# Kernel tuning notes

Hardware: AMD Instinct MI355X
Metric: run time of the kernel (lower is better)

Reference implementation:

```python
import jax, jax.numpy as jnp
import numpy as np

B, H, I = 16384, 512, 256
EPS = 1e-8

def setup_inputs() -> dict:
    key = jax.random.key(0)
    ks = jax.random.split(key, 10)
    x = jax.random.normal(ks[0], (B, I), dtype=jnp.float32)
    hx_re = jax.random.normal(ks[1], (B, H), dtype=jnp.float32) * 0.05
    hx_im = jax.random.normal(ks[2], (B, H), dtype=jnp.float32) * 0.05
    # diag = exp(1j * U(-pi, pi)) -> store angles as real params
    diag_angles = jax.random.uniform(ks[3], (3 * H,), dtype=jnp.float32,
                                     minval=-np.pi, maxval=np.pi)
    # rotation = U(0,1)*2 - (1+1j): real part in [-1,1], imag part in [-1,1]
    rot_re = jax.random.uniform(ks[4], (2 * H,), dtype=jnp.float32) * 2.0 - 1.0
    rot_im = jax.random.uniform(ks[5], (2 * H,), dtype=jnp.float32) * 2.0 - 1.0
    # xavier-scale complex Linear weight (hidden, input), no bias
    w_scale = float(np.sqrt(2.0 / (I + H)))
    W_re = jax.random.normal(ks[6], (H, I), dtype=jnp.float32) * w_scale
    W_im = jax.random.normal(ks[7], (H, I), dtype=jnp.float32) * w_scale
    beta = jnp.zeros((H,), dtype=jnp.float32)  # ModReLU bias, zeros init
    perm = jax.random.permutation(ks[8], H).astype(jnp.int32)
    return {"x": x, "hx_re": hx_re, "hx_im": hx_im,
            "diag_angles": diag_angles, "rot_re": rot_re, "rot_im": rot_im,
            "W_re": W_re, "W_im": W_im, "beta": beta, "perm": perm}

def _unit(v):
    # complex_unit_norm: v / (||v|| + eps), norm over last dim
    return v / (jnp.linalg.norm(v) + EPS)

def _apply_householder(h, v):
    # h @ (I - 2 v v^H) == h - 2 (h @ v) v^H  (rank-1 form, no NxN matrix)
    return h - 2.0 * (h @ v)[:, None] * jnp.conj(v)[None, :]

def reference(x, hx_re, hx_im, diag_angles, rot_re, rot_im, W_re, W_im, beta, perm):
    diag = jnp.exp(1j * diag_angles)                 # complex64, |.| = 1
    d1, d2, d3 = jnp.split(diag, 3)
    rot = rot_re + 1j * rot_im
    r1, r2 = jnp.split(rot, 2)
    v1 = _unit(r1)
    v2 = _unit(r2)

    h = hx_re + 1j * hx_im                           # (B, H) complex64
    h = jnp.fft.fft(d1[None, :] * h, axis=-1)        # D1 then F
    h = _apply_householder(h, v1)                    # R1
    h = jnp.fft.ifft(d2[None, :] * h[:, perm], axis=-1)  # Pi, D2, F^-1
    h = d3[None, :] * _apply_householder(h, v2)      # R2 then D3
    # complex Linear on real input: x @ W^T with complex W
    emb = (x @ W_re.T) + 1j * (x @ W_im.T)
    h = h + emb
    # ModReLU: relu(|z| + beta) * exp(1j * angle(z))
    mag = jnp.abs(h)
    out = jax.nn.relu(mag + beta[None, :]) * jnp.exp(1j * jnp.angle(h))
    # return as real (B, H, 2) [real, imag] for real-valued harness
    return jnp.stack([out.real, out.imag], axis=-1)
```

## Files before the change

kernel.cpp:

```cpp
#include <hip/hip_runtime.h>
#include <hip/hip_bf16.h>
#include <stdint.h>
#include <stddef.h>

typedef __bf16 bf16;
typedef bf16 bf16x8 __attribute__((ext_vector_type(8)));
typedef float f32x4 __attribute__((ext_vector_type(4)));

#define EPSN 1e-8f
#define TWO_PI 6.283185307179586f

#define NB 16384
#define NH 512
#define NI 256
#define KTOT 1280
#define NKT 20

__device__ __forceinline__ float2 cmul(float2 a, float2 b) {
  return make_float2(a.x * b.x - a.y * b.y, a.x * b.y + a.y * b.x);
}
__device__ __forceinline__ float2 cmulconj(float2 a, float2 b) {
  return make_float2(a.x * b.x + a.y * b.y, a.y * b.x - a.x * b.y);
}
__device__ __forceinline__ float2 cadd(float2 a, float2 b) {
  return make_float2(a.x + b.x, a.y + b.y);
}
__device__ __forceinline__ int brev9(int i) {
  return (int)(__brev((unsigned)i) >> 23);
}

__device__ __forceinline__ void gload16(const bf16* g, bf16* l) {
  __builtin_amdgcn_global_load_lds(
      (const __attribute__((address_space(1))) void*)g,
      (__attribute__((address_space(3))) void*)l, 16, 0, 0);
}

__global__ __launch_bounds__(256) void prep(
    const float* __restrict__ ang, const float* __restrict__ rre,
    const float* __restrict__ rim, const float* __restrict__ wre,
    const float* __restrict__ wim, const int* __restrict__ perm,
    const float* __restrict__ hxre, const float* __restrict__ hxim,
    const float* __restrict__ x, bf16* __restrict__ Bm,
    bf16* __restrict__ Apack) {
  __shared__ float2 bufA[512];
  __shared__ float2 bufB[512];
  __shared__ float2 redw[4];
  __shared__ float2 bc;
  __shared__ float2 red2[256];

  const int bid = blockIdx.x;
  const int t = threadIdx.x;

  if (bid >= 512) {
    const int tid = (bid - 512) * 256 + t;
    const int b = tid / 160;
    const int o = tid - b * 160;
    const float* src;
    if (o < 64)
      src = hxre + (size_t)b * 512 + o * 8;
    else if (o < 128)
      src = hxim + (size_t)b * 512 + (o - 64) * 8;
    else
      src = x + (size_t)b * 256 + (o - 128) * 8;
    float4 f0 = ((const float4*)src)[0];
    float4 f1 = ((const float4*)src)[1];
    bf16x8 v;
    v[0] = (bf16)f0.x; v[1] = (bf16)f0.y; v[2] = (bf16)f0.z; v[3] = (bf16)f0.w;
    v[4] = (bf16)f1.x; v[5] = (bf16)f1.y; v[6] = (bf16)f1.z; v[7] = (bf16)f1.w;
    *(bf16x8*)(Apack + (size_t)b * KTOT + o * 8) = v;
    return;
  }

  const int j = bid;
  const int j0 = t, j1 = t + 256;

  const float r1x0 = rre[j0], r1y0 = rim[j0];
  const float r1x1 = rre[j1], r1y1 = rim[j1];
  const float r2x0 = rre[512 + j0], r2y0 = rim[512 + j0];
  const float r2x1 = rre[512 + j1], r2y1 = rim[512 + j1];
  red2[t] = make_float2(r1x0 * r1x0 + r1y0 * r1y0 + r1x1 * r1x1 + r1y1 * r1y1,
                        r2x0 * r2x0 + r2y0 * r2y0 + r2x1 * r2x1 + r2y1 * r2y1);
  __syncthreads();
  for (int off = 128; off > 0; off >>= 1) {
    if (t < off) {
      red2[t].x += red2[t + off].x;
      red2[t].y += red2[t + off].y;
    }
    __syncthreads();
  }
  const float inv1 = 1.0f / (sqrtf(red2[0].x) + EPSN);
  const float inv2 = 1.0f / (sqrtf(red2[0].y) + EPSN);
  const float2 v1a = make_float2(r1x0 * inv1, r1y0 * inv1);
  const float2 v1b = make_float2(r1x1 * inv1, r1y1 * inv1);
  const float2 v2a = make_float2(r2x0 * inv2, r2y0 * inv2);
  const float2 v2b = make_float2(r2x1 * inv2, r2y1 * inv2);

  {
    float sj, cj;
    __sincosf(ang[j], &sj, &cj);
    const float2 dj = make_float2(cj, sj);
    float2 z = make_float2(0.f, 0.f);
    bufA[brev9(j0)] = (j0 == j) ? dj : z;
    bufA[brev9(j1)] = (j1 == j) ? dj : z;
  }
  __syncthreads();

#pragma unroll
  for (int st = 0; st < 9; ++st) {
    const int half = 1 << st;
    const int pos = t & (half - 1);
    const int i0 = ((t >> st) << (st + 1)) + pos;
    const int i1 = i0 + half;
    const float angv = -TWO_PI * (float)pos / (float)(2 << st);
    float sn, cs;
    __sincosf(angv, &sn, &cs);
    float2 u = bufA[i0];
    float2 w = bufA[i1];
    float2 tw = make_float2(cs * w.x - sn * w.y, cs * w.y + sn * w.x);
    bufA[i0] = make_float2(u.x + tw.x, u.y + tw.y);
    bufA[i1] = make_float2(u.x - tw.x, u.y - tw.y);
    __syncthreads();
  }

  {
    float2 p = cadd(cmul(bufA[j0], v1a), cmul(bufA[j1], v1b));
    for (int off = 32; off > 0; off >>= 1) {
      p.x += __shfl_down(p.x, off);
      p.y += __shfl_down(p.y, off);
    }
    if ((t & 63) == 0) redw[t >> 6] = p;
    __syncthreads();
    if (t == 0) bc = cadd(cadd(redw[0], redw[1]), cadd(redw[2], redw[3]));
    __syncthreads();
  }
  const float2 dot1 = bc;

  {
    float2 c0 = cmulconj(dot1, v1a);
    float2 c1 = cmulconj(dot1, v1b);
    float2 a0 = bufA[j0], a1 = bufA[j1];
    bufA[j0] = make_float2(a0.x - 2.f * c0.x, a0.y - 2.f * c0.y);
    bufA[j1] = make_float2(a1.x - 2.f * c1.x, a1.y - 2.f * c1.y);
  }
  __syncthreads();

  {
    int p0 = perm[j0], p1 = perm[j1];
    float s0, c0, s1, c1;
    __sincosf(ang[512 + j0], &s0, &c0);
    __sincosf(ang[512 + j1], &s1, &c1);
    float2 g0 = cmul(make_float2(c0, s0), bufA[p0]);
    float2 g1 = cmul(make_float2(c1, s1), bufA[p1]);
    bufB[brev9(j0)] = g0;
    bufB[brev9(j1)] = g1;
  }
  __syncthreads();

#pragma unroll
  for (int st = 0; st < 9; ++st) {
    const int half = 1 << st;
    const int pos = t & (half - 1);
    const int i0 = ((t >> st) << (st + 1)) + pos;
    const int i1 = i0 + half;
    const float angv = TWO_PI * (float)pos / (float)(2 << st);
    float sn, cs;
    __sincosf(angv, &sn, &cs);
    float2 u = bufB[i0];
    float2 w = bufB[i1];
    float2 tw = make_float2(cs * w.x - sn * w.y, cs * w.y + sn * w.x);
    bufB[i0] = make_float2(u.x + tw.x, u.y + tw.y);
    bufB[i1] = make_float2(u.x - tw.x, u.y - tw.y);
    __syncthreads();
  }

  {
    float2 q = cadd(cmul(bufB[j0], v2a), cmul(bufB[j1], v2b));
    for (int off = 32; off > 0; off >>= 1) {
      q.x += __shfl_down(q.x, off);
      q.y += __shfl_down(q.y, off);
    }
    if ((t & 63) == 0) redw[t >> 6] = q;
    __syncthreads();
    if (t == 0) bc = cadd(cadd(redw[0], redw[1]), cadd(redw[2], redw[3]));
    __syncthreads();
  }
  const float invN = 1.0f / 512.0f;
  const float2 dot2 = make_float2(bc.x * invN, bc.y * invN);

#pragma unroll
  for (int e = 0; e < 2; ++e) {
    const int i = (e == 0) ? j0 : j1;
    const float2 vj = (e == 0) ? v2a : v2b;
    float2 h2 = make_float2(bufB[i].x * invN, bufB[i].y * invN);
    float2 c2 = cmulconj(dot2, vj);
    float2 hh = make_float2(h2.x - 2.f * c2.x, h2.y - 2.f * c2.y);
    float s3, c3;
    __sincosf(ang[1024 + i], &s3, &c3);
    float2 u = cmul(make_float2(c3, s3), hh);
    bf16* r0 = Bm + (size_t)(2 * i) * KTOT;
    bf16* r1 = Bm + (size_t)(2 * i + 1) * KTOT;
    r0[j] = (bf16)u.x;
    r0[512 + j] = (bf16)(-u.y);
    r1[j] = (bf16)u.y;
    r1[512 + j] = (bf16)u.x;
  }

  Bm[(size_t)(2 * j) * KTOT + 1024 + t] = (bf16)wre[j * NI + t];
  Bm[(size_t)(2 * j + 1) * KTOT + 1024 + t] = (bf16)wim[j * NI + t];
}


#define BARM() __builtin_amdgcn_s_barrier()
#define WVM(n) asm volatile("s_waitcnt vmcnt(" #n ")" ::: "memory")

__device__ __forceinline__ void stA(const bf16* gA, bf16* Asb, int wv, int h,
                                    int kt) {
  const int r0 = h * 64 + wv * 8;
  const int r1 = r0 + 128;
  gload16(gA + (size_t)r0 * KTOT + kt * 64, Asb + r0 * 64);
  gload16(gA + (size_t)r1 * KTOT + kt * 64, Asb + r1 * 64);
}
__device__ __forceinline__ void stB(const bf16* gB, bf16* Bsb, int wv, int h,
                                    int kt) {
  const int u0 = wv * 2, u1 = u0 + 1;
  const int r0 = (u0 >> 2) * 64 + h * 32 + (u0 & 3) * 8;
  const int r1 = (u1 >> 2) * 64 + h * 32 + (u1 & 3) * 8;
  gload16(gB + (size_t)r0 * KTOT + kt * 64, Bsb + r0 * 64);
  gload16(gB + (size_t)r1 * KTOT + kt * 64, Bsb + r1 * 64);
}

__device__ __forceinline__ void lda(const bf16* Asb, int rowbase,
                                    const int (&co)[2], bf16x8 (&af)[4][2]) {
#pragma unroll
  for (int mi = 0; mi < 4; ++mi)
#pragma unroll
    for (int kh = 0; kh < 2; ++kh)
      af[mi][kh] = *(const bf16x8*)&Asb[(rowbase + mi * 16) * 64 + co[kh]];
}
__device__ __forceinline__ void ldb(const bf16* Bsb, int rowbase,
                                    const int (&co)[2], bf16x8 (&bb)[2][2]) {
#pragma unroll
  for (int ni = 0; ni < 2; ++ni)
#pragma unroll
    for (int kh = 0; kh < 2; ++kh)
      bb[ni][kh] = *(const bf16x8*)&Bsb[(rowbase + ni * 16) * 64 + co[kh]];
}
__device__ __forceinline__ void mmq(const bf16x8 (&af)[4][2],
                                    const bf16x8 (&bb)[2][2],
                                    f32x4 (&acc)[8][4], int mh, int nh) {
  __builtin_amdgcn_s_setprio(1);
#pragma unroll
  for (int kh = 0; kh < 2; ++kh)
#pragma unroll
    for (int mi = 0; mi < 4; ++mi)
#pragma unroll
      for (int ni = 0; ni < 2; ++ni)
        acc[mh * 4 + mi][nh * 2 + ni] = __builtin_amdgcn_mfma_f32_16x16x32_bf16(
            af[mi][kh], bb[ni][kh], acc[mh * 4 + mi][nh * 2 + ni], 0, 0, 0);
  __builtin_amdgcn_s_setprio(0);
}

__global__ __launch_bounds__(512, 2) void gemm_fused(
    const bf16* __restrict__ Apack, const bf16* __restrict__ Bm,
    const float* __restrict__ beta, float* __restrict__ out) {
  __shared__ bf16 As[2][256 * 64];
  __shared__ bf16 Bs[2][256 * 64];

  const int t = threadIdx.x;
  const int lane = t & 63;
  const int wv = t >> 6;

  const int id = blockIdx.x;
  const int xcd = id & 7;
  const int lix = id >> 3;
  const int mBase = (xcd * 8 + (lix >> 2)) * 256;
  const int nBase = (lix & 3) * 256;

  const int sub = lane >> 3;
  const int chunk = (lane & 7) ^ sub;
  const bf16* gA = Apack + (size_t)(mBase + sub) * KTOT + chunk * 8;
  const bf16* gB = Bm + (size_t)(nBase + sub) * KTOT + chunk * 8;

  const int lr = lane & 15;
  const int lq = lane >> 4;
  const int lrm = lr & 7;
  const int waveM = wv & 1;
  const int waveN = wv >> 1;

  const int co[2] = {(lq ^ lrm) * 8, ((4 + lq) ^ lrm) * 8};
  const int arow = waveM * 128 + lr;
  const int brow = waveN * 64 + lr;

  f32x4 acc[8][4] = {};
  bf16x8 af[4][2], b0[2][2], b1[2][2];

  bf16* As0 = &As[0][0];
  bf16* As1 = &As[1][0];
  bf16* Bs0 = &Bs[0][0];
  bf16* Bs1 = &Bs[1][0];

  stA(gA, As0, wv, 0, 0);
  stB(gB, Bs0, wv, 0, 0);
  stA(gA, As0, wv, 1, 0);
  stB(gB, Bs0, wv, 1, 0);
  stA(gA, As1, wv, 0, 1);
  stB(gB, Bs1, wv, 0, 1);
  WVM(4);
  BARM();
  lda(As0, arow, co, af);
  ldb(Bs0, brow, co, b0);
  stA(gA, As1, wv, 1, 1);
  BARM();

  for (int i = 0; i < 10; ++i) {
    const int T1 = 2 * i + 1;
    const int t2 = (T1 + 1 < NKT) ? T1 + 1 : NKT - 1;
    const int t3 = (T1 + 2 < NKT) ? T1 + 2 : NKT - 1;

    mmq(af, b0, acc, 0, 0);
    ldb(Bs0, brow + 32, co, b1);
    stB(gB, Bs1, wv, 1, T1);
    BARM();
    mmq(af, b1, acc, 0, 1);
    lda(As0, arow + 64, co, af);
    stA(gA, As0, wv, 0, t2);
    BARM();
    mmq(af, b0, acc, 1, 0);
    stB(gB, Bs0, wv, 0, t2);
    WVM(4);
    BARM();
    mmq(af, b1, acc, 1, 1);
    lda(As1, arow, co, af);
    ldb(Bs1, brow, co, b0);
    stA(gA, As0, wv, 1, t2);
    BARM();
    mmq(af, b0, acc, 0, 0);
    ldb(Bs1, brow + 32, co, b1);
    stB(gB, Bs0, wv, 1, t2);
    BARM();
    mmq(af, b1, acc, 0, 1);
    lda(As1, arow + 64, co, af);
    stA(gA, As1, wv, 0, t3);
    BARM();
    mmq(af, b0, acc, 1, 0);
    stB(gB, Bs1, wv, 0, t3);
    WVM(4);
    BARM();
    mmq(af, b1, acc, 1, 1);
    lda(As0, arow, co, af);
    ldb(Bs0, brow, co, b0);
    stA(gA, As1, wv, 1, t3);
    BARM();
  }
  WVM(0);

  const int col = lane & 15;
  const int row0 = lq * 4;
  const int parity = lane & 1;
#pragma unroll
  for (int nq = 0; nq < 4; ++nq) {
    const int n = nBase + waveN * 64 + nq * 16 + col;
    const float bet = beta[n >> 1];
#pragma unroll
    for (int mq = 0; mq < 8; ++mq) {
      const int mrow = mBase + waveM * 128 + mq * 16 + row0;
#pragma unroll
      for (int r = 0; r < 4; ++r) {
        float a = acc[mq][nq][r];
        float o = __shfl_xor(a, 1);
        float re = parity ? o : a;
        float im = parity ? a : o;
        float mag2 = re * re + im * im;
        float val;
        if (mag2 > 0.f) {
          float rs = __frsqrt_rn(mag2);
          float s = mag2 * rs + bet;
          val = (s > 0.f) ? (parity ? im : re) * (s * rs) : 0.f;
        } else {
          val = (bet > 0.f && parity == 0) ? bet : 0.f;
        }
        out[(size_t)(mrow + r) * 1024 + n] = val;
      }
    }
  }
}

extern "C" void kernel_launch(void* const* d_in, const int* in_sizes, int n_in,
                              void* d_out, int out_size, void* d_ws,
                              size_t ws_size, hipStream_t stream) {
  const float* x = (const float*)d_in[0];
  const float* hxre = (const float*)d_in[1];
  const float* hxim = (const float*)d_in[2];
  const float* ang = (const float*)d_in[3];
  const float* rre = (const float*)d_in[4];
  const float* rim = (const float*)d_in[5];
  const float* wre = (const float*)d_in[6];
  const float* wim = (const float*)d_in[7];
  const float* beta = (const float*)d_in[8];
  const int* perm = (const int*)d_in[9];

  char* ws = (char*)d_ws;
  bf16* Bm = (bf16*)ws;
  bf16* Apack = (bf16*)(ws + (size_t)1024 * KTOT * 2);

  prep<<<512 + (NB * 160) / 256, 256, 0, stream>>>(ang, rre, rim, wre, wim,
                                                   perm, hxre, hxim, x, Bm,
                                                   Apack);
  gemm_fused<<<256, 512, 0, stream>>>(Apack, Bm, beta, (float*)d_out);
}
```

Baseline: 201.3 us.

## Stage epilogue through LDS for coalesced stores and add MFMA/DS sched groups

The GEMM epilogue now writes ModReLU results into a shared-memory buffer aliased over the A/B tiles, one 128-row half at a time, and then each wave writes full contiguous rows as float4 stores. Previously each lane stored scattered 4-byte values. The change also inserts sched_group_barrier hints that interleave MFMA and LDS-read instructions before each barrier in the main loop. The cost is extra barriers and an LDS round trip in the epilogue, plus scheduling constraints that may not suit the compiler's own ordering.

```diff
diff --git a/kernel.cpp b/kernel.cpp
--- a/kernel.cpp
+++ b/kernel.cpp
@@ -213,6 +213,14 @@
 #define BARM() __builtin_amdgcn_s_barrier()
 #define WVM(n) asm volatile("s_waitcnt vmcnt(" #n ")" ::: "memory")
 
+__device__ __forceinline__ void IL() {
+#pragma unroll
+  for (int g = 0; g < 8; ++g) {
+    __builtin_amdgcn_sched_group_barrier(0x008, 2, 0);
+    __builtin_amdgcn_sched_group_barrier(0x100, 2, 0);
+  }
+}
+
 __device__ __forceinline__ void stA(const bf16* gA, bf16* Asb, int wv, int h,
                                     int kt) {
   const int r0 = h * 64 + wv * 8;
@@ -263,8 +271,12 @@
 __global__ __launch_bounds__(512, 2) void gemm_fused(
     const bf16* __restrict__ Apack, const bf16* __restrict__ Bm,
     const float* __restrict__ beta, float* __restrict__ out) {
-  __shared__ bf16 As[2][256 * 64];
-  __shared__ bf16 Bs[2][256 * 64];
+  __shared__ __attribute__((aligned(16))) unsigned char SM[131072];
+  bf16* As0 = (bf16*)SM;
+  bf16* As1 = (bf16*)(SM + 32768);
+  bf16* Bs0 = (bf16*)(SM + 65536);
+  bf16* Bs1 = (bf16*)(SM + 98304);
+  float* fbuf = (float*)SM;
 
   const int t = threadIdx.x;
   const int lane = t & 63;
@@ -293,11 +305,6 @@
 
   f32x4 acc[8][4] = {};
   bf16x8 af[4][2], b0[2][2], b1[2][2];
-
-  bf16* As0 = &As[0][0];
-  bf16* As1 = &As[1][0];
-  bf16* Bs0 = &Bs[0][0];
-  bf16* Bs1 = &Bs[1][0];
 
   stA(gA, As0, wv, 0, 0);
   stB(gB, Bs0, wv, 0, 0);
@@ -320,10 +327,12 @@
     mmq(af, b0, acc, 0, 0);
     ldb(Bs0, brow + 32, co, b1);
     stB(gB, Bs1, wv, 1, T1);
+    IL();
     BARM();
     mmq(af, b1, acc, 0, 1);
     lda(As0, arow + 64, co, af);
     stA(gA, As0, wv, 0, t2);
+    IL();
     BARM();
     mmq(af, b0, acc, 1, 0);
     stB(gB, Bs0, wv, 0, t2);
@@ -333,14 +342,17 @@
     lda(As1, arow, co, af);
     ldb(Bs1, brow, co, b0);
     stA(gA, As0, wv, 1, t2);
+    IL();
     BARM();
     mmq(af, b0, acc, 0, 0);
     ldb(Bs1, brow + 32, co, b1);
     stB(gB, Bs0, wv, 1, t2);
+    IL();
     BARM();
     mmq(af, b1, acc, 0, 1);
     lda(As1, arow + 64, co, af);
     stA(gA, As1, wv, 0, t3);
+    IL();
     BARM();
     mmq(af, b0, acc, 1, 0);
     stB(gB, Bs1, wv, 0, t3);
@@ -350,37 +362,50 @@
     lda(As0, arow, co, af);
     ldb(Bs0, brow, co, b0);
     stA(gA, As1, wv, 1, t3);
+    IL();
     BARM();
   }
   WVM(0);
+  BARM();
 
   const int col = lane & 15;
-  const int row0 = lq * 4;
   const int parity = lane & 1;
 #pragma unroll
-  for (int nq = 0; nq < 4; ++nq) {
-    const int n = nBase + waveN * 64 + nq * 16 + col;
-    const float bet = beta[n >> 1];
-#pragma unroll
-    for (int mq = 0; mq < 8; ++mq) {
-      const int mrow = mBase + waveM * 128 + mq * 16 + row0;
-#pragma unroll
-      for (int r = 0; r < 4; ++r) {
-        float a = acc[mq][nq][r];
-        float o = __shfl_xor(a, 1);
-        float re = parity ? o : a;
-        float im = parity ? a : o;
-        float mag2 = re * re + im * im;
-        float val;
-        if (mag2 > 0.f) {
-          float rs = __frsqrt_rn(mag2);
-          float s = mag2 * rs + bet;
-          val = (s > 0.f) ? (parity ? im : re) * (s * rs) : 0.f;
-        } else {
-          val = (bet > 0.f && parity == 0) ? bet : 0.f;
+  for (int half = 0; half < 2; ++half) {
+    if (half) BARM();
+    if (waveM == half) {
+#pragma unroll
+      for (int nq = 0; nq < 4; ++nq) {
+        const int cbase = waveN * 64 + nq * 16 + col;
+        const float bet = beta[(nBase + cbase) >> 1];
+#pragma unroll
+        for (int mq = 0; mq < 8; ++mq) {
+#pragma unroll
+          for (int r = 0; r < 4; ++r) {
+            float a = acc[mq][nq][r];
+            float o = __shfl_xor(a, 1);
+            float re = parity ? o : a;
+            float im = parity ? a : o;
+            float mag2 = re * re + im * im;
+            float val;
+            if (mag2 > 0.f) {
+              float rs = __frsqrt_rn(mag2);
+              float s = mag2 * rs + bet;
+              val = (s > 0.f) ? (parity ? im : re) * (s * rs) : 0.f;
+            } else {
+              val = (bet > 0.f && parity == 0) ? bet : 0.f;
+            }
+            fbuf[(mq * 16 + lq * 4 + r) * 256 + cbase] = val;
+          }
         }
-        out[(size_t)(mrow + r) * 1024 + n] = val;
       }
+    }
+    BARM();
+#pragma unroll
+    for (int rr = 0; rr < 16; ++rr) {
+      const int row = wv * 16 + rr;
+      const float4 v = ((const float4*)(fbuf + row * 256))[lane];
+      ((float4*)(out + (size_t)(mBase + half * 128 + row) * 1024 + nBase))[lane] = v;
     }
   }
 }
```

New measurement: 200.5 us. No clear change (-0.4%).
